# Kernel optimization log

Hardware: AMD Instinct MI355X
Metric: run time of the kernel (lower is better)

The kernel has to match this reference:

```python
import jax, jax.numpy as jnp
import numpy as np

EMBED_DIM = 1024
NUM_HEADS = 16
HEAD_DIM = EMBED_DIM // NUM_HEADS
B, S = 2, 2048


def setup_inputs() -> dict:
    key = jax.random.key(0)
    ks = jax.random.split(key, 10)
    inp = {
        "query": jax.random.normal(ks[0], (B, S, EMBED_DIM), dtype=jnp.float32),
        "key": jax.random.normal(ks[1], (B, S, EMBED_DIM), dtype=jnp.float32),
        "value": jax.random.normal(ks[2], (B, S, EMBED_DIM), dtype=jnp.float32),
        # 0 => masked key position (matches attn_mask == 0 in the torch code)
        "attn_mask": jax.random.randint(ks[3], (B, S), 0, 2, dtype=jnp.int32),
        "Wq": jax.random.normal(ks[4], (EMBED_DIM, EMBED_DIM), dtype=jnp.float32) * 0.02,
        "bq": jnp.zeros((EMBED_DIM,), dtype=jnp.float32),
        "Wk": jax.random.normal(ks[5], (EMBED_DIM, EMBED_DIM), dtype=jnp.float32) * 0.02,
        "bk": jnp.zeros((EMBED_DIM,), dtype=jnp.float32),
        "Wv": jax.random.normal(ks[6], (EMBED_DIM, EMBED_DIM), dtype=jnp.float32) * 0.02,
        "bv": jnp.zeros((EMBED_DIM,), dtype=jnp.float32),
    }
    return inp


def _proj_heads(x, W, b):
    # x: [B, S, E] -> [B, H, S, D]  (nn.Linear uses x @ W.T + b)
    y = x @ W.T + b
    Bx, Sx, E = y.shape
    return y.reshape(Bx, Sx, NUM_HEADS, HEAD_DIM).transpose(0, 2, 1, 3)


def reference(query, key, value, attn_mask, Wq, bq, Wk, bk, Wv, bv):
    q = _proj_heads(query, Wq, bq)   # [B,H,S,D]
    k = _proj_heads(key, Wk, bk)     # [B,H,S,D]
    v = _proj_heads(value, Wv, bv)   # [B,H,S,D]
    inv_scale = float(EMBED_DIM) ** 0.5  # NOTE: original divides by sqrt(embed_dim), not sqrt(head_dim)
    scores = jnp.einsum("bhqd,bhkd->bhqk", q, k) / inv_scale  # [B,H,S,S]
    mask = (attn_mask == 0)[:, None, None, :]  # [B,1,1,S] -> broadcast over [B,H,S,S]
    scores = jnp.where(mask, -jnp.inf, scores)
    attn = jax.nn.softmax(scores, axis=-1)
    # dropout omitted for deterministic reference (see notes)
    out = jnp.einsum("bhqk,bhkd->bhqd", attn, v)  # [B,H,S,D]
    return out
```

## Files before the change

kernel.cpp:

```cpp
#include <hip/hip_runtime.h>
#include <hip/hip_bf16.h>

constexpr int BB = 2;
constexpr int SS = 2048;
constexpr int EE = 1024;
constexpr int HH = 16;
constexpr int DD = 64;
constexpr int MM = BB * SS;
constexpr int CX = MM * EE;
constexpr int CW = EE * EE;
#define QSCALE 0.045084220027780106f
#define NEGBIG -1e30f

typedef __attribute__((ext_vector_type(8))) short short8;
typedef __attribute__((ext_vector_type(4))) float floatx4;

__device__ inline short bf16bits(float x) {
    __hip_bfloat16 h = __float2bfloat16(x);
    return *reinterpret_cast<short*>(&h);
}

__device__ inline unsigned pkbf(float a, float b) {
    return (unsigned)(unsigned short)bf16bits(a) |
           ((unsigned)(unsigned short)bf16bits(b) << 16);
}

__device__ inline float fast_exp2(float x) {
#if __has_builtin(__builtin_amdgcn_exp2f)
    return __builtin_amdgcn_exp2f(x);
#else
    return exp2f(x);
#endif
}

__device__ inline void gl_lds16(const __hip_bfloat16* g, const short* l) {
    __builtin_amdgcn_global_load_lds(
        (const __attribute__((address_space(1))) void*)g,
        (__attribute__((address_space(3))) void*)l, 16, 0, 0);
}

__global__ __launch_bounds__(256) void convert_kernel(
    const float* __restrict__ x0, const float* __restrict__ x1, const float* __restrict__ x2,
    const float* __restrict__ w0, const float* __restrict__ w1, const float* __restrict__ w2,
    __hip_bfloat16* __restrict__ xb, __hip_bfloat16* __restrict__ wb)
{
    const long long e = (long long)(blockIdx.x * 256 + threadIdx.x) * 8;
    const float* src;
    __hip_bfloat16* dst;
    if (e < 3LL * CX) {
        const int z = (int)(e >> 22);
        const int off = (int)(e & (CX - 1));
        src = ((z == 0) ? x0 : (z == 1) ? x1 : x2) + off;
        dst = xb + e;
    } else {
        const long long e2 = e - 3LL * CX;
        const int z = (int)(e2 >> 20);
        const int off = (int)(e2 & (CW - 1));
        src = ((z == 0) ? w0 : (z == 1) ? w1 : w2) + off;
        dst = wb + e2;
    }
    const float4 a = reinterpret_cast<const float4*>(src)[0];
    const float4 b = reinterpret_cast<const float4*>(src)[1];
    short8 r;
    r[0] = bf16bits(a.x); r[1] = bf16bits(a.y); r[2] = bf16bits(a.z); r[3] = bf16bits(a.w);
    r[4] = bf16bits(b.x); r[5] = bf16bits(b.y); r[6] = bf16bits(b.z); r[7] = bf16bits(b.w);
    *reinterpret_cast<short8*>(dst) = r;
}

__global__ __launch_bounds__(256) void proj_gemm(
    const __hip_bfloat16* __restrict__ xb,
    const __hip_bfloat16* __restrict__ wb,
    const float* __restrict__ bq, const float* __restrict__ bk, const float* __restrict__ bv,
    __hip_bfloat16* __restrict__ qws,
    __hip_bfloat16* __restrict__ kws,
    __hip_bfloat16* __restrict__ vtws)
{
    const int which = blockIdx.z;
    const __hip_bfloat16* A = xb + (size_t)which * CX;
    const __hip_bfloat16* W = wb + (size_t)which * CW;
    const float* bias = (which == 0) ? bq : (which == 1) ? bk : bv;

    const int m0   = blockIdx.x * 128;
    const int n0   = blockIdx.y * 128;
    const int tid  = threadIdx.x;
    const int wave = tid >> 6;
    const int lane = tid & 63;
    const int l15  = lane & 15;
    const int quad = lane >> 4;
    const int wr   = wave >> 1;
    const int wc   = wave & 1;

    __shared__ __align__(16) short As[128 * 32];
    __shared__ __align__(16) short Bs[128 * 32];

    const int dpos  = (lane & 7) ^ (lane >> 3);
    const int drloc = 2 * (lane >> 3) + (dpos >> 2);
    const int dgran = (dpos & 3) * 8;

    const int srw   = l15 >> 1;
    const int rbase = (l15 >> 1) * 64;
    const int rslot = (((l15 & 1) * 4 + quad) ^ srw) * 8;

    floatx4 acc[4][4] = {};

    for (int k0 = 0; k0 < EE; k0 += 32) {
        __syncthreads();
        #pragma unroll
        for (int p = 0; p < 2; ++p) {
            const int rb16 = wave * 32 + p * 16;
            gl_lds16(A + (size_t)(m0 + rb16 + drloc) * EE + k0 + dgran, &As[rb16 * 32]);
            gl_lds16(W + (size_t)(n0 + rb16 + drloc) * EE + k0 + dgran, &Bs[rb16 * 32]);
        }
        __syncthreads();

        short8 af[4], bf[4];
        #pragma unroll
        for (int mt = 0; mt < 4; ++mt)
            af[mt] = *reinterpret_cast<const short8*>(
                &As[(wr * 32 + mt * 8) * 64 + rbase + rslot]);
        #pragma unroll
        for (int nt = 0; nt < 4; ++nt)
            bf[nt] = *reinterpret_cast<const short8*>(
                &Bs[(wc * 32 + nt * 8) * 64 + rbase + rslot]);

        #pragma unroll
        for (int mt = 0; mt < 4; ++mt)
            #pragma unroll
            for (int nt = 0; nt < 4; ++nt)
                acc[mt][nt] = __builtin_amdgcn_mfma_f32_16x16x32_bf16(af[mt], bf[nt], acc[mt][nt], 0, 0, 0);
    }

    #pragma unroll
    for (int nt = 0; nt < 4; ++nt) {
        const int n = n0 + wc * 64 + nt * 16 + l15;
        const float bval = bias[n];
        const int h = n >> 6, d = n & 63;
        #pragma unroll
        for (int mt = 0; mt < 4; ++mt) {
            #pragma unroll
            for (int r = 0; r < 4; ++r) {
                const int m = m0 + wr * 64 + mt * 16 + quad * 4 + r;
                const int b = m >> 11;
                const int s = m & (SS - 1);
                float val = acc[mt][nt][r] + bval;
                if (which == 0) val *= QSCALE;
                const __hip_bfloat16 hv = __float2bfloat16(val);
                if (which == 0)
                    qws[(((size_t)b * HH + h) * SS + s) * DD + d] = hv;
                else if (which == 1)
                    kws[(((size_t)b * HH + h) * SS + s) * DD + d] = hv;
                else
                    vtws[(((size_t)b * HH + h) * DD + d) * SS + s] = hv;
            }
        }
    }
}

__global__ __launch_bounds__(256) void attn_kernel(
    const __hip_bfloat16* __restrict__ qws,
    const __hip_bfloat16* __restrict__ kws,
    const __hip_bfloat16* __restrict__ vtws,
    const int* __restrict__ amask,
    float* __restrict__ out)
{
    const int bh   = blockIdx.y;
    const int b    = bh >> 4;
    const int q0   = blockIdx.x * 64;
    const int tid  = threadIdx.x;
    const int wave = tid >> 6;
    const int lane = tid & 63;
    const int l15  = lane & 15;
    const int quad = lane >> 4;

    const __hip_bfloat16* Q  = qws  + (size_t)bh * SS * DD;
    const __hip_bfloat16* K  = kws  + (size_t)bh * SS * DD;
    const __hip_bfloat16* VT = vtws + (size_t)bh * DD * SS;
    const int* msk = amask + b * SS;

    __shared__ __align__(16) short Ks[64 * 64];
    __shared__ __align__(16) short Vs[64 * 64];
    __shared__ __align__(16) short Ps[4][16 * 64];
    short* pw = Ps[wave];

    const int qrow = q0 + wave * 16 + l15;
    const short8 qa0 = *reinterpret_cast<const short8*>(Q + (size_t)qrow * DD + quad * 8);
    const short8 qa1 = *reinterpret_cast<const short8*>(Q + (size_t)qrow * DD + 32 + quad * 8);

    const int swz = l15 & 7;

    float l_lane = 0.f;
    floatx4 acc[4] = {};

    for (int kt = 0; kt < SS; kt += 64) {
        __syncthreads();

        #pragma unroll
        for (int p = 0; p < 2; ++p) {
            const int flat = tid + p * 256;
            const int row = flat >> 3;
            const int g   = flat & 7;
            const int slot = g ^ (row & 7);
            *reinterpret_cast<short8*>(Ks + row * 64 + slot * 8) =
                *reinterpret_cast<const short8*>(K + (size_t)(kt + row) * DD + g * 8);
            *reinterpret_cast<short8*>(Vs + row * 64 + slot * 8) =
                *reinterpret_cast<const short8*>(VT + (size_t)row * SS + kt + g * 8);
        }
        __syncthreads();

        floatx4 st[4];
        #pragma unroll
        for (int f = 0; f < 4; ++f) {
            const int krow = (f * 16 + l15) * 64;
            const short8 ka = *reinterpret_cast<const short8*>(&Ks[krow + (quad ^ swz) * 8]);
            const short8 kb = *reinterpret_cast<const short8*>(&Ks[krow + ((quad + 4) ^ swz) * 8]);
            floatx4 z = {};
            z = __builtin_amdgcn_mfma_f32_16x16x32_bf16(ka, qa0, z, 0, 0, 0);
            z = __builtin_amdgcn_mfma_f32_16x16x32_bf16(kb, qa1, z, 0, 0, 0);
            st[f] = z;
        }

        #pragma unroll
        for (int f = 0; f < 4; ++f) {
            const int4 mi = *reinterpret_cast<const int4*>(msk + kt + f * 16 + quad * 4);
            st[f][0] = fast_exp2(st[f][0] + (mi.x ? 0.f : NEGBIG));
            st[f][1] = fast_exp2(st[f][1] + (mi.y ? 0.f : NEGBIG));
            st[f][2] = fast_exp2(st[f][2] + (mi.z ? 0.f : NEGBIG));
            st[f][3] = fast_exp2(st[f][3] + (mi.w ? 0.f : NEGBIG));
            l_lane += st[f][0] + st[f][1] + st[f][2] + st[f][3];
        }

        #pragma unroll
        for (int f = 0; f < 4; ++f) {
            const int slot = (2 * f + (quad >> 1)) ^ swz;
            uint2 pk;
            pk.x = pkbf(st[f][0], st[f][1]);
            pk.y = pkbf(st[f][2], st[f][3]);
            *reinterpret_cast<uint2*>(pw + l15 * 64 + slot * 8 + (quad & 1) * 4) = pk;
        }
        __asm__ volatile("s_waitcnt lgkmcnt(0)" ::: "memory");

        const short8 pa0 = *reinterpret_cast<const short8*>(pw + l15 * 64 + (quad ^ swz) * 8);
        const short8 pa1 = *reinterpret_cast<const short8*>(pw + l15 * 64 + ((quad + 4) ^ swz) * 8);

        #pragma unroll
        for (int nt = 0; nt < 4; ++nt) {
            const int vrow = (nt * 16 + l15) * 64;
            const short8 vb0 = *reinterpret_cast<const short8*>(&Vs[vrow + (quad ^ swz) * 8]);
            const short8 vb1 = *reinterpret_cast<const short8*>(&Vs[vrow + ((quad + 4) ^ swz) * 8]);
            acc[nt] = __builtin_amdgcn_mfma_f32_16x16x32_bf16(pa0, vb0, acc[nt], 0, 0, 0);
            acc[nt] = __builtin_amdgcn_mfma_f32_16x16x32_bf16(pa1, vb1, acc[nt], 0, 0, 0);
        }
    }

    l_lane += __shfl_xor(l_lane, 16, 64);
    l_lane += __shfl_xor(l_lane, 32, 64);
    float lq[4];
    #pragma unroll
    for (int r = 0; r < 4; ++r)
        lq[r] = __shfl(l_lane, quad * 4 + r, 16);

    const size_t obase = (size_t)bh * SS * DD;
    #pragma unroll
    for (int nt = 0; nt < 4; ++nt)
        #pragma unroll
        for (int r = 0; r < 4; ++r) {
            const int qq = q0 + wave * 16 + quad * 4 + r;
            const int d  = nt * 16 + l15;
            out[obase + (size_t)qq * DD + d] = acc[nt][r] / lq[r];
        }
}

extern "C" void kernel_launch(void* const* d_in, const int* in_sizes, int n_in,
                              void* d_out, int out_size, void* d_ws, size_t ws_size,
                              hipStream_t stream) {
    const float* q    = (const float*)d_in[0];
    const float* k    = (const float*)d_in[1];
    const float* v    = (const float*)d_in[2];
    const int*   mask = (const int*)d_in[3];
    const float* Wq   = (const float*)d_in[4];
    const float* bq   = (const float*)d_in[5];
    const float* Wk   = (const float*)d_in[6];
    const float* bk   = (const float*)d_in[7];
    const float* Wv   = (const float*)d_in[8];
    const float* bv   = (const float*)d_in[9];
    float* out = (float*)d_out;

    __hip_bfloat16* qws  = (__hip_bfloat16*)d_ws;
    __hip_bfloat16* kws  = qws + (size_t)CX;
    __hip_bfloat16* vtws = kws + (size_t)CX;
    __hip_bfloat16* xb   = vtws + (size_t)CX;
    __hip_bfloat16* wb   = xb + (size_t)3 * CX;

    const int cvt_blocks = (3 * CX + 3 * CW) / (256 * 8);
    convert_kernel<<<dim3(cvt_blocks), 256, 0, stream>>>(q, k, v, Wq, Wk, Wv, xb, wb);
    proj_gemm<<<dim3(MM / 128, EE / 128, 3), 256, 0, stream>>>(
        xb, wb, bq, bk, bv, qws, kws, vtws);
    attn_kernel<<<dim3(SS / 64, BB * HH), 256, 0, stream>>>(
        qws, kws, vtws, mask, out);
}
```

Measured before the change: 218.5 us.

## Use single-wave 64x64 tiles with double-buffered async LDS loads in projection GEMM

The projection GEMM moves from a 256-thread block computing a 128x128 tile to a one-wave block computing a 64x64 tile. Because each block is a single wave, both __syncthreads calls go away. Two LDS buffers are added, so the next K-slice is loaded while the current one is used, with s_waitcnt vmcnt controlling completion. The aim is to hide global-load latency and remove barrier stalls, at the cost of less tile reuse across waves, more global/L2 traffic and four times as many blocks.

```diff
diff --git a/kernel.cpp b/kernel.cpp
--- a/kernel.cpp
+++ b/kernel.cpp
@@ -67,7 +67,7 @@
     *reinterpret_cast<short8*>(dst) = r;
 }
 
-__global__ __launch_bounds__(256) void proj_gemm(
+__global__ __launch_bounds__(64) void proj_gemm(
     const __hip_bfloat16* __restrict__ xb,
     const __hip_bfloat16* __restrict__ wb,
     const float* __restrict__ bq, const float* __restrict__ bk, const float* __restrict__ bv,
@@ -80,48 +80,51 @@
     const __hip_bfloat16* W = wb + (size_t)which * CW;
     const float* bias = (which == 0) ? bq : (which == 1) ? bk : bv;
 
-    const int m0   = blockIdx.x * 128;
-    const int n0   = blockIdx.y * 128;
-    const int tid  = threadIdx.x;
-    const int wave = tid >> 6;
-    const int lane = tid & 63;
+    const int m0   = blockIdx.x * 64;
+    const int n0   = blockIdx.y * 64;
+    const int lane = threadIdx.x;
     const int l15  = lane & 15;
     const int quad = lane >> 4;
-    const int wr   = wave >> 1;
-    const int wc   = wave & 1;
-
-    __shared__ __align__(16) short As[128 * 32];
-    __shared__ __align__(16) short Bs[128 * 32];
+
+    __shared__ __align__(16) short As[2][64 * 32];
+    __shared__ __align__(16) short Bs[2][64 * 32];
 
     const int dpos  = (lane & 7) ^ (lane >> 3);
     const int drloc = 2 * (lane >> 3) + (dpos >> 2);
     const int dgran = (dpos & 3) * 8;
 
-    const int srw   = l15 >> 1;
     const int rbase = (l15 >> 1) * 64;
-    const int rslot = (((l15 & 1) * 4 + quad) ^ srw) * 8;
+    const int rslot = (((l15 & 1) * 4 + quad) ^ (l15 >> 1)) * 8;
 
     floatx4 acc[4][4] = {};
 
-    for (int k0 = 0; k0 < EE; k0 += 32) {
-        __syncthreads();
-        #pragma unroll
-        for (int p = 0; p < 2; ++p) {
-            const int rb16 = wave * 32 + p * 16;
-            gl_lds16(A + (size_t)(m0 + rb16 + drloc) * EE + k0 + dgran, &As[rb16 * 32]);
-            gl_lds16(W + (size_t)(n0 + rb16 + drloc) * EE + k0 + dgran, &Bs[rb16 * 32]);
-        }
-        __syncthreads();
+    auto issue = [&](int k0, int buf) {
+        #pragma unroll
+        for (int p = 0; p < 4; ++p) {
+            const int rb16 = p * 16;
+            gl_lds16(A + (size_t)(m0 + rb16 + drloc) * EE + k0 + dgran, &As[buf][rb16 * 32]);
+            gl_lds16(W + (size_t)(n0 + rb16 + drloc) * EE + k0 + dgran, &Bs[buf][rb16 * 32]);
+        }
+    };
+
+    issue(0, 0);
+
+    for (int t = 0; t < EE / 32; ++t) {
+        const int buf = t & 1;
+        if (t + 1 < EE / 32) {
+            issue((t + 1) * 32, buf ^ 1);
+            __asm__ volatile("s_waitcnt vmcnt(8)" ::: "memory");
+        } else {
+            __asm__ volatile("s_waitcnt vmcnt(0)" ::: "memory");
+        }
 
         short8 af[4], bf[4];
         #pragma unroll
         for (int mt = 0; mt < 4; ++mt)
-            af[mt] = *reinterpret_cast<const short8*>(
-                &As[(wr * 32 + mt * 8) * 64 + rbase + rslot]);
+            af[mt] = *reinterpret_cast<const short8*>(&As[buf][(mt * 8) * 64 + rbase + rslot]);
         #pragma unroll
         for (int nt = 0; nt < 4; ++nt)
-            bf[nt] = *reinterpret_cast<const short8*>(
-                &Bs[(wc * 32 + nt * 8) * 64 + rbase + rslot]);
+            bf[nt] = *reinterpret_cast<const short8*>(&Bs[buf][(nt * 8) * 64 + rbase + rslot]);
 
         #pragma unroll
         for (int mt = 0; mt < 4; ++mt)
@@ -132,14 +135,14 @@
 
     #pragma unroll
     for (int nt = 0; nt < 4; ++nt) {
-        const int n = n0 + wc * 64 + nt * 16 + l15;
+        const int n = n0 + nt * 16 + l15;
         const float bval = bias[n];
         const int h = n >> 6, d = n & 63;
         #pragma unroll
         for (int mt = 0; mt < 4; ++mt) {
             #pragma unroll
             for (int r = 0; r < 4; ++r) {
-                const int m = m0 + wr * 64 + mt * 16 + quad * 4 + r;
+                const int m = m0 + mt * 16 + quad * 4 + r;
                 const int b = m >> 11;
                 const int s = m & (SS - 1);
                 float val = acc[mt][nt][r] + bval;
@@ -293,7 +296,7 @@
 
     const int cvt_blocks = (3 * CX + 3 * CW) / (256 * 8);
     convert_kernel<<<dim3(cvt_blocks), 256, 0, stream>>>(q, k, v, Wq, Wk, Wv, xb, wb);
-    proj_gemm<<<dim3(MM / 128, EE / 128, 3), 256, 0, stream>>>(
+    proj_gemm<<<dim3(MM / 64, EE / 64, 3), 64, 0, stream>>>(
         xb, wb, bq, bk, bv, qws, kws, vtws);
     attn_kernel<<<dim3(SS / 64, BB * HH), 256, 0, stream>>>(
         qws, kws, vtws, mask, out);
```

New measurement: 242.0 us. 1.11x slower.

## Process two 16-row query groups per wave in attention to reuse K/V tiles

Applied to the files above, without the earlier changes.

Each attention block now handles 128 query rows instead of 64, with every wave computing two 16-row query groups against the same K and V tiles loaded into shared memory. This halves the number of K/V global loads and LDS fills per query row and gives each wave more MFMA work between barriers. In exchange the grid drops to 512 blocks, which may lower occupancy and latency hiding, and register and LDS use per block rise. A small inline cleanup of a swizzle variable in the projection GEMM is included.

```diff
diff --git a/kernel.cpp b/kernel.cpp
--- a/kernel.cpp
+++ b/kernel.cpp
@@ -97,9 +97,8 @@
     const int drloc = 2 * (lane >> 3) + (dpos >> 2);
     const int dgran = (dpos & 3) * 8;
 
-    const int srw   = l15 >> 1;
     const int rbase = (l15 >> 1) * 64;
-    const int rslot = (((l15 & 1) * 4 + quad) ^ srw) * 8;
+    const int rslot = (((l15 & 1) * 4 + quad) ^ (l15 >> 1)) * 8;
 
     floatx4 acc[4][4] = {};
 
@@ -165,7 +164,7 @@
 {
     const int bh   = blockIdx.y;
     const int b    = bh >> 4;
-    const int q0   = blockIdx.x * 64;
+    const int q0   = blockIdx.x * 128;
     const int tid  = threadIdx.x;
     const int wave = tid >> 6;
     const int lane = tid & 63;
@@ -179,17 +178,21 @@
 
     __shared__ __align__(16) short Ks[64 * 64];
     __shared__ __align__(16) short Vs[64 * 64];
-    __shared__ __align__(16) short Ps[4][16 * 64];
+    __shared__ __align__(16) short Ps[4][2 * 16 * 64];
     short* pw = Ps[wave];
 
-    const int qrow = q0 + wave * 16 + l15;
-    const short8 qa0 = *reinterpret_cast<const short8*>(Q + (size_t)qrow * DD + quad * 8);
-    const short8 qa1 = *reinterpret_cast<const short8*>(Q + (size_t)qrow * DD + 32 + quad * 8);
+    short8 qa[2][2];
+    #pragma unroll
+    for (int g = 0; g < 2; ++g) {
+        const int qrow = q0 + wave * 32 + g * 16 + l15;
+        qa[g][0] = *reinterpret_cast<const short8*>(Q + (size_t)qrow * DD + quad * 8);
+        qa[g][1] = *reinterpret_cast<const short8*>(Q + (size_t)qrow * DD + 32 + quad * 8);
+    }
 
     const int swz = l15 & 7;
 
-    float l_lane = 0.f;
-    floatx4 acc[4] = {};
+    float l_lane[2] = {0.f, 0.f};
+    floatx4 acc[2][4] = {};
 
     for (int kt = 0; kt < SS; kt += 64) {
         __syncthreads();
@@ -207,67 +210,89 @@
         }
         __syncthreads();
 
-        floatx4 st[4];
+        floatx4 st[2][4];
         #pragma unroll
         for (int f = 0; f < 4; ++f) {
             const int krow = (f * 16 + l15) * 64;
             const short8 ka = *reinterpret_cast<const short8*>(&Ks[krow + (quad ^ swz) * 8]);
             const short8 kb = *reinterpret_cast<const short8*>(&Ks[krow + ((quad + 4) ^ swz) * 8]);
-            floatx4 z = {};
-            z = __builtin_amdgcn_mfma_f32_16x16x32_bf16(ka, qa0, z, 0, 0, 0);
-            z = __builtin_amdgcn_mfma_f32_16x16x32_bf16(kb, qa1, z, 0, 0, 0);
-            st[f] = z;
+            #pragma unroll
+            for (int g = 0; g < 2; ++g) {
+                floatx4 z = {};
+                z = __builtin_amdgcn_mfma_f32_16x16x32_bf16(ka, qa[g][0], z, 0, 0, 0);
+                z = __builtin_amdgcn_mfma_f32_16x16x32_bf16(kb, qa[g][1], z, 0, 0, 0);
+                st[g][f] = z;
+            }
         }
 
         #pragma unroll
         for (int f = 0; f < 4; ++f) {
             const int4 mi = *reinterpret_cast<const int4*>(msk + kt + f * 16 + quad * 4);
-            st[f][0] = fast_exp2(st[f][0] + (mi.x ? 0.f : NEGBIG));
-            st[f][1] = fast_exp2(st[f][1] + (mi.y ? 0.f : NEGBIG));
-            st[f][2] = fast_exp2(st[f][2] + (mi.z ? 0.f : NEGBIG));
-            st[f][3] = fast_exp2(st[f][3] + (mi.w ? 0.f : NEGBIG));
-            l_lane += st[f][0] + st[f][1] + st[f][2] + st[f][3];
-        }
-
-        #pragma unroll
-        for (int f = 0; f < 4; ++f) {
-            const int slot = (2 * f + (quad >> 1)) ^ swz;
-            uint2 pk;
-            pk.x = pkbf(st[f][0], st[f][1]);
-            pk.y = pkbf(st[f][2], st[f][3]);
-            *reinterpret_cast<uint2*>(pw + l15 * 64 + slot * 8 + (quad & 1) * 4) = pk;
-        }
+            const float b0 = mi.x ? 0.f : NEGBIG;
+            const float b1 = mi.y ? 0.f : NEGBIG;
+            const float b2 = mi.z ? 0.f : NEGBIG;
+            const float b3 = mi.w ? 0.f : NEGBIG;
+            #pragma unroll
+            for (int g = 0; g < 2; ++g) {
+                st[g][f][0] = fast_exp2(st[g][f][0] + b0);
+                st[g][f][1] = fast_exp2(st[g][f][1] + b1);
+                st[g][f][2] = fast_exp2(st[g][f][2] + b2);
+                st[g][f][3] = fast_exp2(st[g][f][3] + b3);
+                l_lane[g] += st[g][f][0] + st[g][f][1] + st[g][f][2] + st[g][f][3];
+            }
+        }
+
+        #pragma unroll
+        for (int g = 0; g < 2; ++g)
+            #pragma unroll
+            for (int f = 0; f < 4; ++f) {
+                const int slot = (2 * f + (quad >> 1)) ^ swz;
+                uint2 pk;
+                pk.x = pkbf(st[g][f][0], st[g][f][1]);
+                pk.y = pkbf(st[g][f][2], st[g][f][3]);
+                *reinterpret_cast<uint2*>(pw + g * 1024 + l15 * 64 + slot * 8 + (quad & 1) * 4) = pk;
+            }
         __asm__ volatile("s_waitcnt lgkmcnt(0)" ::: "memory");
 
-        const short8 pa0 = *reinterpret_cast<const short8*>(pw + l15 * 64 + (quad ^ swz) * 8);
-        const short8 pa1 = *reinterpret_cast<const short8*>(pw + l15 * 64 + ((quad + 4) ^ swz) * 8);
+        short8 pa[2][2];
+        #pragma unroll
+        for (int g = 0; g < 2; ++g) {
+            pa[g][0] = *reinterpret_cast<const short8*>(pw + g * 1024 + l15 * 64 + (quad ^ swz) * 8);
+            pa[g][1] = *reinterpret_cast<const short8*>(pw + g * 1024 + l15 * 64 + ((quad + 4) ^ swz) * 8);
+        }
 
         #pragma unroll
         for (int nt = 0; nt < 4; ++nt) {
             const int vrow = (nt * 16 + l15) * 64;
             const short8 vb0 = *reinterpret_cast<const short8*>(&Vs[vrow + (quad ^ swz) * 8]);
             const short8 vb1 = *reinterpret_cast<const short8*>(&Vs[vrow + ((quad + 4) ^ swz) * 8]);
-            acc[nt] = __builtin_amdgcn_mfma_f32_16x16x32_bf16(pa0, vb0, acc[nt], 0, 0, 0);
-            acc[nt] = __builtin_amdgcn_mfma_f32_16x16x32_bf16(pa1, vb1, acc[nt], 0, 0, 0);
-        }
-    }
-
-    l_lane += __shfl_xor(l_lane, 16, 64);
-    l_lane += __shfl_xor(l_lane, 32, 64);
-    float lq[4];
-    #pragma unroll
-    for (int r = 0; r < 4; ++r)
-        lq[r] = __shfl(l_lane, quad * 4 + r, 16);
+            #pragma unroll
+            for (int g = 0; g < 2; ++g) {
+                acc[g][nt] = __builtin_amdgcn_mfma_f32_16x16x32_bf16(pa[g][0], vb0, acc[g][nt], 0, 0, 0);
+                acc[g][nt] = __builtin_amdgcn_mfma_f32_16x16x32_bf16(pa[g][1], vb1, acc[g][nt], 0, 0, 0);
+            }
+        }
+    }
 
     const size_t obase = (size_t)bh * SS * DD;
     #pragma unroll
-    for (int nt = 0; nt < 4; ++nt)
-        #pragma unroll
-        for (int r = 0; r < 4; ++r) {
-            const int qq = q0 + wave * 16 + quad * 4 + r;
-            const int d  = nt * 16 + l15;
-            out[obase + (size_t)qq * DD + d] = acc[nt][r] / lq[r];
-        }
+    for (int g = 0; g < 2; ++g) {
+        float lg = l_lane[g];
+        lg += __shfl_xor(lg, 16, 64);
+        lg += __shfl_xor(lg, 32, 64);
+        float lq[4];
+        #pragma unroll
+        for (int r = 0; r < 4; ++r)
+            lq[r] = __shfl(lg, quad * 4 + r, 16);
+        #pragma unroll
+        for (int nt = 0; nt < 4; ++nt)
+            #pragma unroll
+            for (int r = 0; r < 4; ++r) {
+                const int qq = q0 + wave * 32 + g * 16 + quad * 4 + r;
+                const int d  = nt * 16 + l15;
+                out[obase + (size_t)qq * DD + d] = acc[g][nt][r] / lq[r];
+            }
+    }
 }
 
 extern "C" void kernel_launch(void* const* d_in, const int* in_sizes, int n_in,
@@ -295,6 +320,6 @@
     convert_kernel<<<dim3(cvt_blocks), 256, 0, stream>>>(q, k, v, Wq, Wk, Wv, xb, wb);
     proj_gemm<<<dim3(MM / 128, EE / 128, 3), 256, 0, stream>>>(
         xb, wb, bq, bk, bv, qws, kws, vtws);
-    attn_kernel<<<dim3(SS / 64, BB * HH), 256, 0, stream>>>(
+    attn_kernel<<<dim3(SS / 128, BB * HH), 256, 0, stream>>>(
         qws, kws, vtws, mask, out);
 }
```

Result: slower. 250.3 us (+14.5%).
